# Kernel tuning notes

Measured on AMD Instinct MI355X. Metric: run time of the kernel, lower is better.

Reference implementation:

```python
import jax, jax.numpy as jnp
import numpy as np

N_Q = 4  # QuantumSampler is hard-wired to 4 qubits (16-dim statevector)


def _build_tables():
    """Static permutation for the CNOT chain and Z-sign table, computed once in numpy."""
    n = N_Q
    dim = 1 << n
    cnots = [(i, (i + 1) % n) for i in range(n)]  # (0,1),(1,2),(2,3),(3,0)
    fmap = np.empty(dim, dtype=np.int64)
    for i in range(dim):
        bits = [(i >> (n - 1 - w)) & 1 for w in range(n)]  # wire w <-> bit (n-1-w)
        for c, t in cnots:
            if bits[c]:
                bits[t] ^= 1
        fmap[i] = sum(b << (n - 1 - w) for w, b in enumerate(bits))
    finv = np.argsort(fmap)  # new_state[j] = old_state[finv[j]]
    signs = np.array([[1.0 - 2.0 * ((j >> (n - 1 - w)) & 1) for w in range(n)]
                      for j in range(dim)], dtype=np.float32)  # <Z_w> signs per basis state
    return jnp.asarray(finv), jnp.asarray(signs)

PERM, SIGNS = _build_tables()


def quantum_gate_probs(q, theta):
    """Simulate: RX(q_w) then RX(theta_w) per wire (angles add), CNOT chain, <Z> per wire, softmax.
    q: [B,4] encoder angles; theta: [4] trainable angles. Returns [B,4] gate probabilities."""
    half = 0.5 * (q + theta)                      # RX(a)RX(b) = RX(a+b)
    c = jnp.cos(half).astype(jnp.complex64)       # amplitude on |0>
    s = (jnp.sin(half).astype(jnp.complex64)) * (-1j)  # amplitude on |1> is -i sin(a/2)
    a = jnp.stack([c, s], axis=-1)                # [B,4,2] single-qubit states
    a0, a1, a2, a3 = a[:, 0], a[:, 1], a[:, 2], a[:, 3]
    # product state |psi> = a0 (x) a1 (x) a2 (x) a3  -> [B,2,2,2,2] -> [B,16]
    st = (a0[:, :, None, None, None] * a1[:, None, :, None, None]
          * a2[:, None, None, :, None] * a3[:, None, None, None, :])
    st = st.reshape(q.shape[0], 16)[:, PERM]      # apply CNOT chain (amplitude permutation)
    probs = st.real ** 2 + st.imag ** 2           # [B,16]
    exps = probs @ SIGNS                          # [B,4] Pauli-Z expectations per wire
    return jax.nn.softmax(exps, axis=-1)


def setup_inputs() -> dict:
    key = jax.random.key(0)
    ks = jax.random.split(key, 8)
    T, B, D, H = 256, 128, 1024, 1024
    inputs = jax.random.normal(ks[0], (T, B, D), dtype=jnp.float32)
    sc_d = 1.0 / np.sqrt(D)
    sc_h = 1.0 / np.sqrt(H)
    return {
        "inputs": inputs,
        "Wi": jax.random.normal(ks[1], (H, D), dtype=jnp.float32) * sc_d,
        "bi": jnp.zeros((H,), dtype=jnp.float32),
        "Wh": jax.random.normal(ks[2], (H, H), dtype=jnp.float32) * sc_h,
        "bh": jnp.zeros((H,), dtype=jnp.float32),
        "Wq": jax.random.normal(ks[3], (4, H), dtype=jnp.float32) * sc_h,
        "bq": jnp.zeros((4,), dtype=jnp.float32),
        "theta": jax.random.uniform(ks[4], (4,), dtype=jnp.float32, minval=-np.pi, maxval=np.pi),
    }


def reference(inputs, Wi, bi, Wh, bh, Wq, bq, theta):
    T, B, _ = inputs.shape
    H = Wi.shape[0]
    hx0 = jnp.zeros((B, H), dtype=inputs.dtype)
    cx0 = jnp.zeros((B, H), dtype=inputs.dtype)

    def step(carry, x):
        hx, cx = carry
        combined = x @ Wi.T + bi + hx @ Wh.T + bh   # [B,H]
        qin = combined @ Wq.T + bq                  # [B,4]
        gates = quantum_gate_probs(qin, theta)      # [B,4]
        f, i_, g, o = gates[:, 0:1], gates[:, 1:2], gates[:, 2:3], gates[:, 3:4]
        cx = f * cx + i_ * jnp.tanh(g)              # broadcast [B,1]*[B,H]
        hx = o * jnp.tanh(cx)
        return (hx, cx), hx

    (hx, cx), ys = jax.lax.scan(step, (hx0, cx0), inputs)
    return ys, hx, cx
```

## Files before the change

kernel.cpp:

```cpp
#include <hip/hip_runtime.h>

#define T_STEPS 256
#define BATCH   128
#define DIM     1024
#define NROWS   (T_STEPS * BATCH)
#define TOTROWS (NROWS + 2 * BATCH)

typedef float vfloat4 __attribute__((ext_vector_type(4)));

#define WS_M     0
#define WS_V     4096
#define WS_CB    4128
#define WS_ZERO_BYTES ((WS_CB + 4) * 4)
#define WS_QX    8192
#define WS_HSEQ  (WS_QX + 4 * NROWS)
#define WS_CFIN  (WS_HSEQ + NROWS)

__global__ __launch_bounds__(256) void k_prep(const float* __restrict__ Wi,
                                              const float* __restrict__ Wh,
                                              const float* __restrict__ bi,
                                              const float* __restrict__ bh,
                                              const float* __restrict__ Wq,
                                              float* __restrict__ M,
                                              float* __restrict__ v,
                                              float* __restrict__ cb) {
    int blk  = blockIdx.x;
    int tid  = threadIdx.x;
    int wave = tid >> 6;
    int lane = tid & 63;

    if (blk < 64) {
        int j0 = blk * 16;
        #pragma unroll
        for (int db = 0; db < 4; db++) {
            int d = db * 256 + tid;
            float a0 = 0.f, a1 = 0.f, a2 = 0.f, a3 = 0.f;
            #pragma unroll 4
            for (int jj = 0; jj < 16; jj++) {
                int j = j0 + jj;
                float wv = Wi[(size_t)j * DIM + d];
                a0 += Wq[0 * DIM + j] * wv;
                a1 += Wq[1 * DIM + j] * wv;
                a2 += Wq[2 * DIM + j] * wv;
                a3 += Wq[3 * DIM + j] * wv;
            }
            unsafeAtomicAdd(&M[0 * DIM + d], a0);
            unsafeAtomicAdd(&M[1 * DIM + d], a1);
            unsafeAtomicAdd(&M[2 * DIM + d], a2);
            unsafeAtomicAdd(&M[3 * DIM + d], a3);
        }
    } else {
        int j0 = (blk - 64) * 16 + wave * 4;
        float sv0 = 0.f, sv1 = 0.f, sv2 = 0.f, sv3 = 0.f;
        float sc0 = 0.f, sc1 = 0.f, sc2 = 0.f, sc3 = 0.f;
        #pragma unroll
        for (int jj = 0; jj < 4; jj++) {
            int j = j0 + jj;
            const float4* row = (const float4*)(Wh + (size_t)j * DIM);
            float s = 0.f;
            #pragma unroll
            for (int k = 0; k < 4; k++) {
                float4 t4 = row[k * 64 + lane];
                s += t4.x + t4.y + t4.z + t4.w;
            }
            #pragma unroll
            for (int off = 32; off; off >>= 1) s += __shfl_xor(s, off, 64);
            float bb = bi[j] + bh[j];
            float q0 = Wq[0 * DIM + j], q1 = Wq[1 * DIM + j];
            float q2 = Wq[2 * DIM + j], q3 = Wq[3 * DIM + j];
            sv0 += q0 * s;  sc0 += q0 * bb;
            sv1 += q1 * s;  sc1 += q1 * bb;
            sv2 += q2 * s;  sc2 += q2 * bb;
            sv3 += q3 * s;  sc3 += q3 * bb;
        }
        if (lane == 0) {
            unsafeAtomicAdd(&v[0], sv0);  unsafeAtomicAdd(&v[1], sv1);
            unsafeAtomicAdd(&v[2], sv2);  unsafeAtomicAdd(&v[3], sv3);
            unsafeAtomicAdd(&cb[0], sc0); unsafeAtomicAdd(&cb[1], sc1);
            unsafeAtomicAdd(&cb[2], sc2); unsafeAtomicAdd(&cb[3], sc3);
        }
    }
}

__global__ __launch_bounds__(256) void k_qx(const float* __restrict__ x,
                                            const float* __restrict__ M,
                                            float4* __restrict__ qx4) {
    int gtid   = blockIdx.x * blockDim.x + threadIdx.x;
    int wave   = gtid >> 6;
    int lane   = threadIdx.x & 63;
    int nwaves = (gridDim.x * blockDim.x) >> 6;

    float4 m[4][4];
    #pragma unroll
    for (int w = 0; w < 4; w++)
        #pragma unroll
        for (int k = 0; k < 4; k++)
            m[w][k] = *(const float4*)(M + w * DIM + k * 256 + lane * 4);

    for (int r = wave; r < NROWS; r += nwaves) {
        const float4* row = (const float4*)(x + (size_t)r * DIM);
        float a0 = 0.f, a1 = 0.f, a2 = 0.f, a3 = 0.f;
        #pragma unroll
        for (int k = 0; k < 4; k++) {
            float4 xv = row[k * 64 + lane];
            a0 += xv.x * m[0][k].x + xv.y * m[0][k].y + xv.z * m[0][k].z + xv.w * m[0][k].w;
            a1 += xv.x * m[1][k].x + xv.y * m[1][k].y + xv.z * m[1][k].z + xv.w * m[1][k].w;
            a2 += xv.x * m[2][k].x + xv.y * m[2][k].y + xv.z * m[2][k].z + xv.w * m[2][k].w;
            a3 += xv.x * m[3][k].x + xv.y * m[3][k].y + xv.z * m[3][k].z + xv.w * m[3][k].w;
        }
        #pragma unroll
        for (int off = 32; off; off >>= 1) {
            a0 += __shfl_xor(a0, off, 64);
            a1 += __shfl_xor(a1, off, 64);
            a2 += __shfl_xor(a2, off, 64);
            a3 += __shfl_xor(a3, off, 64);
        }
        if (lane == 0) qx4[r] = make_float4(a0, a1, a2, a3);
    }
}

__device__ __forceinline__ float fast_tanh(float x) {
    float e = __expf(2.f * x);
    return (e - 1.f) * __builtin_amdgcn_rcpf(e + 1.f);
}

__device__ __forceinline__ void rec_step(float4 q,
                                         float b0, float b1, float b2, float b3,
                                         float v0, float v1, float v2, float v3,
                                         float& h, float& c) {
    float z0 = __cosf(q.x + b0 + h * v0);
    float z1 = __cosf(q.y + b1 + h * v1);
    float z2 = __cosf(q.z + b2 + h * v2);
    float z3 = __cosf(q.w + b3 + h * v3);
    float e1 = z0 * z1;
    float e2 = e1 * z2;
    float e3 = e2 * z3;
    float e0 = z1 * z2 * z3;
    float x0 = __expf(e0), x1 = __expf(e1), x2 = __expf(e2), x3 = __expf(e3);
    float inv = __builtin_amdgcn_rcpf(x0 + x1 + x2 + x3);
    float f  = x0 * inv;
    float i_ = x1 * inv;
    float g  = x2 * inv;
    float o  = x3 * inv;
    c = f * c + i_ * fast_tanh(g);
    h = o * fast_tanh(c);
}

__global__ __launch_bounds__(128) void k_rec(const float* __restrict__ bq,
                                             const float* __restrict__ theta,
                                             const float* __restrict__ v,
                                             const float* __restrict__ cbp,
                                             const float4* __restrict__ qx4,
                                             float* __restrict__ hseq,
                                             float* __restrict__ cfin) {
    int b = threadIdx.x;

    float v0 = v[0], v1 = v[1], v2 = v[2], v3 = v[3];
    float b0 = cbp[0] + bq[0] + theta[0];
    float b1 = cbp[1] + bq[1] + theta[1];
    float b2 = cbp[2] + bq[2] + theta[2];
    float b3 = cbp[3] + bq[3] + theta[3];

    float h = 0.f, c = 0.f;

    float4 q0 = qx4[0 * BATCH + b], q1 = qx4[1 * BATCH + b];
    float4 q2 = qx4[2 * BATCH + b], q3 = qx4[3 * BATCH + b];
    float4 q4 = qx4[4 * BATCH + b], q5 = qx4[5 * BATCH + b];
    float4 q6 = qx4[6 * BATCH + b], q7 = qx4[7 * BATCH + b];

    for (int t = 0; t < T_STEPS; t += 8) {
        float4 n0, n1, n2, n3, n4, n5, n6, n7;
        if (t + 8 < T_STEPS) {
            n0 = qx4[(t + 8)  * BATCH + b];  n1 = qx4[(t + 9)  * BATCH + b];
            n2 = qx4[(t + 10) * BATCH + b];  n3 = qx4[(t + 11) * BATCH + b];
            n4 = qx4[(t + 12) * BATCH + b];  n5 = qx4[(t + 13) * BATCH + b];
            n6 = qx4[(t + 14) * BATCH + b];  n7 = qx4[(t + 15) * BATCH + b];
        }
        rec_step(q0, b0, b1, b2, b3, v0, v1, v2, v3, h, c); hseq[(t + 0) * BATCH + b] = h;
        rec_step(q1, b0, b1, b2, b3, v0, v1, v2, v3, h, c); hseq[(t + 1) * BATCH + b] = h;
        rec_step(q2, b0, b1, b2, b3, v0, v1, v2, v3, h, c); hseq[(t + 2) * BATCH + b] = h;
        rec_step(q3, b0, b1, b2, b3, v0, v1, v2, v3, h, c); hseq[(t + 3) * BATCH + b] = h;
        rec_step(q4, b0, b1, b2, b3, v0, v1, v2, v3, h, c); hseq[(t + 4) * BATCH + b] = h;
        rec_step(q5, b0, b1, b2, b3, v0, v1, v2, v3, h, c); hseq[(t + 5) * BATCH + b] = h;
        rec_step(q6, b0, b1, b2, b3, v0, v1, v2, v3, h, c); hseq[(t + 6) * BATCH + b] = h;
        rec_step(q7, b0, b1, b2, b3, v0, v1, v2, v3, h, c); hseq[(t + 7) * BATCH + b] = h;
        q0 = n0; q1 = n1; q2 = n2; q3 = n3; q4 = n4; q5 = n5; q6 = n6; q7 = n7;
    }
    cfin[b] = c;
}

__global__ __launch_bounds__(256) void k_write(const float* __restrict__ hseq,
                                               const float* __restrict__ cfin,
                                               float* __restrict__ out) {
    int tid  = threadIdx.x;
    int r    = blockIdx.x * 4 + (tid >> 6);
    int lane = tid & 63;

    float val;
    if      (r < NROWS)          val = hseq[r];
    else if (r < NROWS + BATCH)  val = hseq[(T_STEPS - 1) * BATCH + (r - NROWS)];
    else                         val = cfin[r - NROWS - BATCH];

    vfloat4 vv = {val, val, val, val};
    vfloat4* orow = (vfloat4*)(out + (size_t)r * DIM);
    __builtin_nontemporal_store(vv, &orow[0 * 64 + lane]);
    __builtin_nontemporal_store(vv, &orow[1 * 64 + lane]);
    __builtin_nontemporal_store(vv, &orow[2 * 64 + lane]);
    __builtin_nontemporal_store(vv, &orow[3 * 64 + lane]);
}

extern "C" void kernel_launch(void* const* d_in, const int* in_sizes, int n_in,
                              void* d_out, int out_size, void* d_ws, size_t ws_size,
                              hipStream_t stream) {
    const float* inputs = (const float*)d_in[0];
    const float* Wi     = (const float*)d_in[1];
    const float* bi     = (const float*)d_in[2];
    const float* Wh     = (const float*)d_in[3];
    const float* bh     = (const float*)d_in[4];
    const float* Wq     = (const float*)d_in[5];
    const float* bq     = (const float*)d_in[6];
    const float* theta  = (const float*)d_in[7];
    float* out = (float*)d_out;
    float* ws  = (float*)d_ws;

    float*  M    = ws + WS_M;
    float*  v    = ws + WS_V;
    float*  cb   = ws + WS_CB;
    float4* qx4  = (float4*)(ws + WS_QX);
    float*  hseq = ws + WS_HSEQ;
    float*  cfin = ws + WS_CFIN;

    (void)hipMemsetAsync(ws, 0, WS_ZERO_BYTES, stream);
    k_prep <<<128,  256, 0, stream>>>(Wi, Wh, bi, bh, Wq, M, v, cb);
    k_qx   <<<1024, 256, 0, stream>>>(inputs, M, qx4);
    k_rec  <<<1,    128, 0, stream>>>(bq, theta, v, cb, qx4, hseq, cfin);
    k_write<<<TOTROWS / 4, 256, 0, stream>>>(hseq, cfin, out);
}
```

Measured before the change: 314.1 us.

## Fuse all stages into one cooperative kernel with grid syncs

```diff
diff --git a/kernel.cpp b/kernel.cpp
--- a/kernel.cpp
+++ b/kernel.cpp
@@ -1,4 +1,7 @@
 #include <hip/hip_runtime.h>
+#include <hip/hip_cooperative_groups.h>
+
+namespace cg = cooperative_groups;
 
 #define T_STEPS 256
 #define BATCH   128
@@ -11,113 +14,12 @@
 #define WS_M     0
 #define WS_V     4096
 #define WS_CB    4128
-#define WS_ZERO_BYTES ((WS_CB + 4) * 4)
 #define WS_QX    8192
 #define WS_HSEQ  (WS_QX + 4 * NROWS)
 #define WS_CFIN  (WS_HSEQ + NROWS)
-
-__global__ __launch_bounds__(256) void k_prep(const float* __restrict__ Wi,
-                                              const float* __restrict__ Wh,
-                                              const float* __restrict__ bi,
-                                              const float* __restrict__ bh,
-                                              const float* __restrict__ Wq,
-                                              float* __restrict__ M,
-                                              float* __restrict__ v,
-                                              float* __restrict__ cb) {
-    int blk  = blockIdx.x;
-    int tid  = threadIdx.x;
-    int wave = tid >> 6;
-    int lane = tid & 63;
-
-    if (blk < 64) {
-        int j0 = blk * 16;
-        #pragma unroll
-        for (int db = 0; db < 4; db++) {
-            int d = db * 256 + tid;
-            float a0 = 0.f, a1 = 0.f, a2 = 0.f, a3 = 0.f;
-            #pragma unroll 4
-            for (int jj = 0; jj < 16; jj++) {
-                int j = j0 + jj;
-                float wv = Wi[(size_t)j * DIM + d];
-                a0 += Wq[0 * DIM + j] * wv;
-                a1 += Wq[1 * DIM + j] * wv;
-                a2 += Wq[2 * DIM + j] * wv;
-                a3 += Wq[3 * DIM + j] * wv;
-            }
-            unsafeAtomicAdd(&M[0 * DIM + d], a0);
-            unsafeAtomicAdd(&M[1 * DIM + d], a1);
-            unsafeAtomicAdd(&M[2 * DIM + d], a2);
-            unsafeAtomicAdd(&M[3 * DIM + d], a3);
-        }
-    } else {
-        int j0 = (blk - 64) * 16 + wave * 4;
-        float sv0 = 0.f, sv1 = 0.f, sv2 = 0.f, sv3 = 0.f;
-        float sc0 = 0.f, sc1 = 0.f, sc2 = 0.f, sc3 = 0.f;
-        #pragma unroll
-        for (int jj = 0; jj < 4; jj++) {
-            int j = j0 + jj;
-            const float4* row = (const float4*)(Wh + (size_t)j * DIM);
-            float s = 0.f;
-            #pragma unroll
-            for (int k = 0; k < 4; k++) {
-                float4 t4 = row[k * 64 + lane];
-                s += t4.x + t4.y + t4.z + t4.w;
-            }
-            #pragma unroll
-            for (int off = 32; off; off >>= 1) s += __shfl_xor(s, off, 64);
-            float bb = bi[j] + bh[j];
-            float q0 = Wq[0 * DIM + j], q1 = Wq[1 * DIM + j];
-            float q2 = Wq[2 * DIM + j], q3 = Wq[3 * DIM + j];
-            sv0 += q0 * s;  sc0 += q0 * bb;
-            sv1 += q1 * s;  sc1 += q1 * bb;
-            sv2 += q2 * s;  sc2 += q2 * bb;
-            sv3 += q3 * s;  sc3 += q3 * bb;
-        }
-        if (lane == 0) {
-            unsafeAtomicAdd(&v[0], sv0);  unsafeAtomicAdd(&v[1], sv1);
-            unsafeAtomicAdd(&v[2], sv2);  unsafeAtomicAdd(&v[3], sv3);
-            unsafeAtomicAdd(&cb[0], sc0); unsafeAtomicAdd(&cb[1], sc1);
-            unsafeAtomicAdd(&cb[2], sc2); unsafeAtomicAdd(&cb[3], sc3);
-        }
-    }
-}
-
-__global__ __launch_bounds__(256) void k_qx(const float* __restrict__ x,
-                                            const float* __restrict__ M,
-                                            float4* __restrict__ qx4) {
-    int gtid   = blockIdx.x * blockDim.x + threadIdx.x;
-    int wave   = gtid >> 6;
-    int lane   = threadIdx.x & 63;
-    int nwaves = (gridDim.x * blockDim.x) >> 6;
-
-    float4 m[4][4];
-    #pragma unroll
-    for (int w = 0; w < 4; w++)
-        #pragma unroll
-        for (int k = 0; k < 4; k++)
-            m[w][k] = *(const float4*)(M + w * DIM + k * 256 + lane * 4);
-
-    for (int r = wave; r < NROWS; r += nwaves) {
-        const float4* row = (const float4*)(x + (size_t)r * DIM);
-        float a0 = 0.f, a1 = 0.f, a2 = 0.f, a3 = 0.f;
-        #pragma unroll
-        for (int k = 0; k < 4; k++) {
-            float4 xv = row[k * 64 + lane];
-            a0 += xv.x * m[0][k].x + xv.y * m[0][k].y + xv.z * m[0][k].z + xv.w * m[0][k].w;
-            a1 += xv.x * m[1][k].x + xv.y * m[1][k].y + xv.z * m[1][k].z + xv.w * m[1][k].w;
-            a2 += xv.x * m[2][k].x + xv.y * m[2][k].y + xv.z * m[2][k].z + xv.w * m[2][k].w;
-            a3 += xv.x * m[3][k].x + xv.y * m[3][k].y + xv.z * m[3][k].z + xv.w * m[3][k].w;
-        }
-        #pragma unroll
-        for (int off = 32; off; off >>= 1) {
-            a0 += __shfl_xor(a0, off, 64);
-            a1 += __shfl_xor(a1, off, 64);
-            a2 += __shfl_xor(a2, off, 64);
-            a3 += __shfl_xor(a3, off, 64);
-        }
-        if (lane == 0) qx4[r] = make_float4(a0, a1, a2, a3);
-    }
-}
+#define WS_MPART (WS_CFIN + 128)
+#define WS_VPART (WS_MPART + 64 * 4096)
+#define WS_CPART (WS_VPART + 256)
 
 __device__ __forceinline__ float fast_tanh(float x) {
     float e = __expf(2.f * x);
@@ -146,67 +48,192 @@
     h = o * fast_tanh(c);
 }
 
-__global__ __launch_bounds__(128) void k_rec(const float* __restrict__ bq,
-                                             const float* __restrict__ theta,
-                                             const float* __restrict__ v,
-                                             const float* __restrict__ cbp,
-                                             const float4* __restrict__ qx4,
-                                             float* __restrict__ hseq,
-                                             float* __restrict__ cfin) {
-    int b = threadIdx.x;
-
-    float v0 = v[0], v1 = v[1], v2 = v[2], v3 = v[3];
-    float b0 = cbp[0] + bq[0] + theta[0];
-    float b1 = cbp[1] + bq[1] + theta[1];
-    float b2 = cbp[2] + bq[2] + theta[2];
-    float b3 = cbp[3] + bq[3] + theta[3];
-
-    float h = 0.f, c = 0.f;
-
-    float4 q0 = qx4[0 * BATCH + b], q1 = qx4[1 * BATCH + b];
-    float4 q2 = qx4[2 * BATCH + b], q3 = qx4[3 * BATCH + b];
-    float4 q4 = qx4[4 * BATCH + b], q5 = qx4[5 * BATCH + b];
-    float4 q6 = qx4[6 * BATCH + b], q7 = qx4[7 * BATCH + b];
-
-    for (int t = 0; t < T_STEPS; t += 8) {
-        float4 n0, n1, n2, n3, n4, n5, n6, n7;
-        if (t + 8 < T_STEPS) {
-            n0 = qx4[(t + 8)  * BATCH + b];  n1 = qx4[(t + 9)  * BATCH + b];
-            n2 = qx4[(t + 10) * BATCH + b];  n3 = qx4[(t + 11) * BATCH + b];
-            n4 = qx4[(t + 12) * BATCH + b];  n5 = qx4[(t + 13) * BATCH + b];
-            n6 = qx4[(t + 14) * BATCH + b];  n7 = qx4[(t + 15) * BATCH + b];
-        }
-        rec_step(q0, b0, b1, b2, b3, v0, v1, v2, v3, h, c); hseq[(t + 0) * BATCH + b] = h;
-        rec_step(q1, b0, b1, b2, b3, v0, v1, v2, v3, h, c); hseq[(t + 1) * BATCH + b] = h;
-        rec_step(q2, b0, b1, b2, b3, v0, v1, v2, v3, h, c); hseq[(t + 2) * BATCH + b] = h;
-        rec_step(q3, b0, b1, b2, b3, v0, v1, v2, v3, h, c); hseq[(t + 3) * BATCH + b] = h;
-        rec_step(q4, b0, b1, b2, b3, v0, v1, v2, v3, h, c); hseq[(t + 4) * BATCH + b] = h;
-        rec_step(q5, b0, b1, b2, b3, v0, v1, v2, v3, h, c); hseq[(t + 5) * BATCH + b] = h;
-        rec_step(q6, b0, b1, b2, b3, v0, v1, v2, v3, h, c); hseq[(t + 6) * BATCH + b] = h;
-        rec_step(q7, b0, b1, b2, b3, v0, v1, v2, v3, h, c); hseq[(t + 7) * BATCH + b] = h;
-        q0 = n0; q1 = n1; q2 = n2; q3 = n3; q4 = n4; q5 = n5; q6 = n6; q7 = n7;
-    }
-    cfin[b] = c;
-}
-
-__global__ __launch_bounds__(256) void k_write(const float* __restrict__ hseq,
-                                               const float* __restrict__ cfin,
-                                               float* __restrict__ out) {
+__global__ __launch_bounds__(256, 1) void k_all(
+        const float* __restrict__ x,   const float* __restrict__ Wi,
+        const float* __restrict__ Wh,  const float* __restrict__ bi,
+        const float* __restrict__ bh,  const float* __restrict__ Wq,
+        const float* __restrict__ bq,  const float* __restrict__ theta,
+        float* __restrict__ out,
+        float* __restrict__ M,     float* __restrict__ v,
+        float* __restrict__ cb,    float4* __restrict__ qx4,
+        float* __restrict__ hseq,  float* __restrict__ cfin,
+        float* __restrict__ Mpart, float* __restrict__ vpart,
+        float* __restrict__ cpart) {
+    cg::grid_group grid = cg::this_grid();
+    int blk  = blockIdx.x;
     int tid  = threadIdx.x;
-    int r    = blockIdx.x * 4 + (tid >> 6);
+    int wave = tid >> 6;
     int lane = tid & 63;
 
-    float val;
-    if      (r < NROWS)          val = hseq[r];
-    else if (r < NROWS + BATCH)  val = hseq[(T_STEPS - 1) * BATCH + (r - NROWS)];
-    else                         val = cfin[r - NROWS - BATCH];
-
-    vfloat4 vv = {val, val, val, val};
-    vfloat4* orow = (vfloat4*)(out + (size_t)r * DIM);
-    __builtin_nontemporal_store(vv, &orow[0 * 64 + lane]);
-    __builtin_nontemporal_store(vv, &orow[1 * 64 + lane]);
-    __builtin_nontemporal_store(vv, &orow[2 * 64 + lane]);
-    __builtin_nontemporal_store(vv, &orow[3 * 64 + lane]);
+    if (blk < 64) {
+        int j0 = blk * 16;
+        float* base = Mpart + (size_t)blk * 4096;
+        #pragma unroll
+        for (int db = 0; db < 4; db++) {
+            int d = db * 256 + tid;
+            float a0 = 0.f, a1 = 0.f, a2 = 0.f, a3 = 0.f;
+            #pragma unroll 4
+            for (int jj = 0; jj < 16; jj++) {
+                int j = j0 + jj;
+                float wv = Wi[(size_t)j * DIM + d];
+                a0 += Wq[0 * DIM + j] * wv;
+                a1 += Wq[1 * DIM + j] * wv;
+                a2 += Wq[2 * DIM + j] * wv;
+                a3 += Wq[3 * DIM + j] * wv;
+            }
+            base[0 * DIM + d] = a0;
+            base[1 * DIM + d] = a1;
+            base[2 * DIM + d] = a2;
+            base[3 * DIM + d] = a3;
+        }
+    } else if (blk < 128) {
+        int bb_ = blk - 64;
+        int j0  = bb_ * 16 + wave * 4;
+        float sv0 = 0.f, sv1 = 0.f, sv2 = 0.f, sv3 = 0.f;
+        float sc0 = 0.f, sc1 = 0.f, sc2 = 0.f, sc3 = 0.f;
+        #pragma unroll
+        for (int jj = 0; jj < 4; jj++) {
+            int j = j0 + jj;
+            const float4* row = (const float4*)(Wh + (size_t)j * DIM);
+            float s = 0.f;
+            #pragma unroll
+            for (int k = 0; k < 4; k++) {
+                float4 t4 = row[k * 64 + lane];
+                s += t4.x + t4.y + t4.z + t4.w;
+            }
+            #pragma unroll
+            for (int off = 32; off; off >>= 1) s += __shfl_xor(s, off, 64);
+            float bsum = bi[j] + bh[j];
+            float q0 = Wq[0 * DIM + j], q1 = Wq[1 * DIM + j];
+            float q2 = Wq[2 * DIM + j], q3 = Wq[3 * DIM + j];
+            sv0 += q0 * s;    sv1 += q1 * s;    sv2 += q2 * s;    sv3 += q3 * s;
+            sc0 += q0 * bsum; sc1 += q1 * bsum; sc2 += q2 * bsum; sc3 += q3 * bsum;
+        }
+        __shared__ float ls[4][8];
+        if (lane == 0) {
+            ls[wave][0] = sv0; ls[wave][1] = sv1; ls[wave][2] = sv2; ls[wave][3] = sv3;
+            ls[wave][4] = sc0; ls[wave][5] = sc1; ls[wave][6] = sc2; ls[wave][7] = sc3;
+        }
+        __syncthreads();
+        if (tid < 8) {
+            float s = ls[0][tid] + ls[1][tid] + ls[2][tid] + ls[3][tid];
+            if (tid < 4) vpart[bb_ * 4 + tid]       = s;
+            else         cpart[bb_ * 4 + (tid - 4)] = s;
+        }
+    }
+    grid.sync();
+
+    if (blk < 16) {
+        int f = blk * 256 + tid;
+        float s = 0.f;
+        #pragma unroll 8
+        for (int jc = 0; jc < 64; jc++) s += Mpart[(size_t)jc * 4096 + f];
+        M[f] = s;
+    } else if (blk == 16 && tid < 8) {
+        const float* src = (tid < 4) ? vpart : cpart;
+        int w = tid & 3;
+        float s = 0.f;
+        #pragma unroll 8
+        for (int jc = 0; jc < 64; jc++) s += src[jc * 4 + w];
+        if (tid < 4) v[w] = s; else cb[w] = s;
+    }
+    grid.sync();
+
+    {
+        float4 m[4][4];
+        #pragma unroll
+        for (int w = 0; w < 4; w++)
+            #pragma unroll
+            for (int k = 0; k < 4; k++)
+                m[w][k] = *(const float4*)(M + w * DIM + k * 256 + lane * 4);
+
+        int r = blk * 4 + wave;
+        float4 cur[4];
+        {
+            const float4* row = (const float4*)(x + (size_t)r * DIM);
+            #pragma unroll
+            for (int k = 0; k < 4; k++) cur[k] = row[k * 64 + lane];
+        }
+        while (r < NROWS) {
+            int rn = r + 1024;
+            float4 nxt[4];
+            if (rn < NROWS) {
+                const float4* nrow = (const float4*)(x + (size_t)rn * DIM);
+                #pragma unroll
+                for (int k = 0; k < 4; k++) nxt[k] = nrow[k * 64 + lane];
+            }
+            float a0 = 0.f, a1 = 0.f, a2 = 0.f, a3 = 0.f;
+            #pragma unroll
+            for (int k = 0; k < 4; k++) {
+                float4 xv = cur[k];
+                a0 += xv.x * m[0][k].x + xv.y * m[0][k].y + xv.z * m[0][k].z + xv.w * m[0][k].w;
+                a1 += xv.x * m[1][k].x + xv.y * m[1][k].y + xv.z * m[1][k].z + xv.w * m[1][k].w;
+                a2 += xv.x * m[2][k].x + xv.y * m[2][k].y + xv.z * m[2][k].z + xv.w * m[2][k].w;
+                a3 += xv.x * m[3][k].x + xv.y * m[3][k].y + xv.z * m[3][k].z + xv.w * m[3][k].w;
+            }
+            #pragma unroll
+            for (int off = 32; off; off >>= 1) {
+                a0 += __shfl_xor(a0, off, 64);
+                a1 += __shfl_xor(a1, off, 64);
+                a2 += __shfl_xor(a2, off, 64);
+                a3 += __shfl_xor(a3, off, 64);
+            }
+            if (lane == 0) qx4[r] = make_float4(a0, a1, a2, a3);
+            #pragma unroll
+            for (int k = 0; k < 4; k++) cur[k] = nxt[k];
+            r = rn;
+        }
+    }
+    grid.sync();
+
+    if (blk == 0 && tid < BATCH) {
+        int b = tid;
+        float v0 = *(volatile const float*)(v + 0);
+        float v1 = *(volatile const float*)(v + 1);
+        float v2 = *(volatile const float*)(v + 2);
+        float v3 = *(volatile const float*)(v + 3);
+        float b0 = *(volatile const float*)(cb + 0) + bq[0] + theta[0];
+        float b1 = *(volatile const float*)(cb + 1) + bq[1] + theta[1];
+        float b2 = *(volatile const float*)(cb + 2) + bq[2] + theta[2];
+        float b3 = *(volatile const float*)(cb + 3) + bq[3] + theta[3];
+
+        float h = 0.f, c = 0.f;
+        float4 q0 = qx4[0 * BATCH + b], q1 = qx4[1 * BATCH + b];
+        float4 q2 = qx4[2 * BATCH + b], q3 = qx4[3 * BATCH + b];
+        float4 q4 = qx4[4 * BATCH + b], q5 = qx4[5 * BATCH + b];
+        float4 q6 = qx4[6 * BATCH + b], q7 = qx4[7 * BATCH + b];
+
+        for (int t = 0; t < T_STEPS; t += 8) {
+            float4 n0, n1, n2, n3, n4, n5, n6, n7;
+            if (t + 8 < T_STEPS) {
+                n0 = qx4[(t + 8)  * BATCH + b];  n1 = qx4[(t + 9)  * BATCH + b];
+                n2 = qx4[(t + 10) * BATCH + b];  n3 = qx4[(t + 11) * BATCH + b];
+                n4 = qx4[(t + 12) * BATCH + b];  n5 = qx4[(t + 13) * BATCH + b];
+                n6 = qx4[(t + 14) * BATCH + b];  n7 = qx4[(t + 15) * BATCH + b];
+            }
+            rec_step(q0, b0, b1, b2, b3, v0, v1, v2, v3, h, c); hseq[(t + 0) * BATCH + b] = h;
+            rec_step(q1, b0, b1, b2, b3, v0, v1, v2, v3, h, c); hseq[(t + 1) * BATCH + b] = h;
+            rec_step(q2, b0, b1, b2, b3, v0, v1, v2, v3, h, c); hseq[(t + 2) * BATCH + b] = h;
+            rec_step(q3, b0, b1, b2, b3, v0, v1, v2, v3, h, c); hseq[(t + 3) * BATCH + b] = h;
+            rec_step(q4, b0, b1, b2, b3, v0, v1, v2, v3, h, c); hseq[(t + 4) * BATCH + b] = h;
+            rec_step(q5, b0, b1, b2, b3, v0, v1, v2, v3, h, c); hseq[(t + 5) * BATCH + b] = h;
+            rec_step(q6, b0, b1, b2, b3, v0, v1, v2, v3, h, c); hseq[(t + 6) * BATCH + b] = h;
+            rec_step(q7, b0, b1, b2, b3, v0, v1, v2, v3, h, c); hseq[(t + 7) * BATCH + b] = h;
+            q0 = n0; q1 = n1; q2 = n2; q3 = n3; q4 = n4; q5 = n5; q6 = n6; q7 = n7;
+        }
+        cfin[b] = c;
+    }
+    grid.sync();
+
+    for (int r = blk; r < TOTROWS; r += 256) {
+        float val;
+        if      (r < NROWS)         val = *(volatile const float*)(hseq + r);
+        else if (r < NROWS + BATCH) val = *(volatile const float*)(hseq + (T_STEPS - 1) * BATCH + (r - NROWS));
+        else                        val = *(volatile const float*)(cfin + (r - NROWS - BATCH));
+        vfloat4 vv = {val, val, val, val};
+        vfloat4* orow = (vfloat4*)(out + (size_t)r * DIM);
+        __builtin_nontemporal_store(vv, &orow[tid]);
+    }
 }
 
 extern "C" void kernel_launch(void* const* d_in, const int* in_sizes, int n_in,
@@ -223,16 +250,19 @@
     float* out = (float*)d_out;
     float* ws  = (float*)d_ws;
 
-    float*  M    = ws + WS_M;
-    float*  v    = ws + WS_V;
-    float*  cb   = ws + WS_CB;
-    float4* qx4  = (float4*)(ws + WS_QX);
-    float*  hseq = ws + WS_HSEQ;
-    float*  cfin = ws + WS_CFIN;
-
-    (void)hipMemsetAsync(ws, 0, WS_ZERO_BYTES, stream);
-    k_prep <<<128,  256, 0, stream>>>(Wi, Wh, bi, bh, Wq, M, v, cb);
-    k_qx   <<<1024, 256, 0, stream>>>(inputs, M, qx4);
-    k_rec  <<<1,    128, 0, stream>>>(bq, theta, v, cb, qx4, hseq, cfin);
-    k_write<<<TOTROWS / 4, 256, 0, stream>>>(hseq, cfin, out);
-}
+    float*  M     = ws + WS_M;
+    float*  v     = ws + WS_V;
+    float*  cb    = ws + WS_CB;
+    float4* qx4   = (float4*)(ws + WS_QX);
+    float*  hseq  = ws + WS_HSEQ;
+    float*  cfin  = ws + WS_CFIN;
+    float*  Mpart = ws + WS_MPART;
+    float*  vpart = ws + WS_VPART;
+    float*  cpart = ws + WS_CPART;
+
+    void* args[] = { &inputs, &Wi, &Wh, &bi, &bh, &Wq, &bq, &theta,
+                     &out, &M, &v, &cb, &qx4, &hseq, &cfin,
+                     &Mpart, &vpart, &cpart };
+    (void)hipLaunchCooperativeKernel((void*)k_all, dim3(256), dim3(256),
+                                     args, 0, stream);
+}
```

New measurement: 443.3 us. 41.1% more time.
